# Kernel tuning notes

Measured on AMD Instinct MI355X. Metric: run time of the kernel, lower is better.

## Reference

```python
import jax, jax.numpy as jnp
import numpy as np

N_HEAD, D_MODEL, D_K, D_V = 16, 1024, 64, 64
B, S = 2, 2048
LN_EPS = 1e-5


def setup_inputs() -> dict:
    key = jax.random.key(0)
    ks = jax.random.split(key, 9)
    std_qk = np.sqrt(2.0 / (D_MODEL + D_K)).astype(np.float32)
    std_v = np.sqrt(2.0 / (D_MODEL + D_V)).astype(np.float32)
    return {
        "q": jax.random.normal(ks[0], (B, S, D_MODEL), jnp.float32),
        "k": jax.random.normal(ks[1], (B, S, D_MODEL), jnp.float32),
        "v": jax.random.normal(ks[2], (B, S, D_MODEL), jnp.float32),
        # nn.Linear weights stored as [out, in]; we apply x @ W.T
        "w_qs": jax.random.normal(ks[3], (N_HEAD * D_K, D_MODEL), jnp.float32) * std_qk,
        "w_ks": jax.random.normal(ks[4], (N_HEAD * D_K, D_MODEL), jnp.float32) * std_qk,
        "w_vs": jax.random.normal(ks[5], (N_HEAD * D_V, D_MODEL), jnp.float32) * std_v,
        "fc_w": jax.random.normal(ks[6], (D_MODEL, N_HEAD * D_V), jnp.float32) * np.sqrt(2.0 / (D_MODEL + N_HEAD * D_V)).astype(np.float32),
        "fc_b": jnp.zeros((D_MODEL,), jnp.float32),
        "ln_g": jnp.ones((D_MODEL,), jnp.float32),
        "ln_b": jnp.zeros((D_MODEL,), jnp.float32),
    }


def reference(q, k, v, w_qs, w_ks, w_vs, fc_w, fc_b, ln_g, ln_b):
    temperature = jnp.asarray(np.power(D_K, 0.5), q.dtype)
    residual = q
    # projections -> [b, s, h, d]
    qh = (q @ w_qs.T).reshape(B, S, N_HEAD, D_K)
    kh = (k @ w_ks.T).reshape(B, S, N_HEAD, D_K)
    vh = (v @ w_vs.T).reshape(B, S, N_HEAD, D_V)
    # scaled dot-product attention (dropout = identity in eval)
    attn = jnp.einsum('bqhd,bkhd->bhqk', qh, kh) / temperature
    attn = jax.nn.softmax(attn, axis=-1)  # (log_softmax in source is unused)
    out = jnp.einsum('bhqk,bkhd->bqhd', attn, vh).reshape(B, S, N_HEAD * D_V)
    out = out @ fc_w.T + fc_b
    # layer norm over last dim
    x = out + residual
    mu = jnp.mean(x, axis=-1, keepdims=True)
    var = jnp.var(x, axis=-1, keepdims=True)
    return (x - mu) * jax.lax.rsqrt(var + LN_EPS) * ln_g + ln_b
```

## Files before the change

### kernel.cpp

```cpp
#include <hip/hip_runtime.h>
#include <hip/hip_bf16.h>

typedef _Float16 f16x8 __attribute__((ext_vector_type(8)));
typedef _Float16 f16x4 __attribute__((ext_vector_type(4)));
typedef _Float16 f16x2 __attribute__((ext_vector_type(2)));
typedef float f32x4 __attribute__((ext_vector_type(4)));

#define DEVI __device__ __forceinline__

constexpr int S_LEN = 2048;
constexpr int DM    = 1024;
constexpr int NH    = 16;
constexpr int DHD   = 64;
constexpr int MTOT  = 2 * S_LEN;

DEVI f32x4 mfma16(f16x8 a, f16x8 b, f32x4 c) {
    return __builtin_amdgcn_mfma_f32_16x16x32_f16(a, b, c, 0, 0, 0);
}

DEVI f16x2 cvt_pk(float a, float b) {
    return __builtin_bit_cast(f16x2, __builtin_amdgcn_cvt_pkrtz(a, b));
}

DEVI float fexp2(float x) {
#if __has_builtin(__builtin_amdgcn_exp2f)
    return __builtin_amdgcn_exp2f(x);
#else
    return exp2f(x);
#endif
}

DEVI void gload_lds16(const _Float16* g, _Float16* l) {
    __builtin_amdgcn_global_load_lds(
        (const __attribute__((address_space(1))) void*)g,
        (__attribute__((address_space(3))) void*)l, 16, 0, 0);
}

__global__ void k_conv(const float* __restrict__ s0, const float* __restrict__ s1,
                       const float* __restrict__ s2, const float* __restrict__ s3,
                       const float* __restrict__ s4, const float* __restrict__ s5,
                       const float* __restrict__ s6,
                       _Float16* __restrict__ d0, _Float16* __restrict__ d1,
                       _Float16* __restrict__ d2, _Float16* __restrict__ d3,
                       _Float16* __restrict__ d4, _Float16* __restrict__ d5,
                       _Float16* __restrict__ d6)
{
    const int QN4 = (MTOT * DM) / 4;
    const int WN4 = (DM * DM) / 4;
    const int TOT = 3 * QN4 + 4 * WN4;
    int stride = gridDim.x * blockDim.x;
    for (int i = blockIdx.x * blockDim.x + threadIdx.x; i < TOT; i += stride) {
        const float* s; _Float16* d; int off;
        if (i < 3 * QN4) {
            int t = i / QN4; off = i - t * QN4;
            s = t == 0 ? s0 : (t == 1 ? s1 : s2);
            d = t == 0 ? d0 : (t == 1 ? d1 : d2);
        } else {
            int j = i - 3 * QN4;
            int t = j / WN4; off = j - t * WN4;
            s = t == 0 ? s3 : (t == 1 ? s4 : (t == 2 ? s5 : s6));
            d = t == 0 ? d3 : (t == 1 ? d4 : (t == 2 ? d5 : d6));
        }
        float4 v = reinterpret_cast<const float4*>(s)[off];
        f16x4 o;
        o[0] = (_Float16)v.x; o[1] = (_Float16)v.y;
        o[2] = (_Float16)v.z; o[3] = (_Float16)v.w;
        *reinterpret_cast<f16x4*>(d + (size_t)off * 4) = o;
    }
}

DEVI void gemm_main(const _Float16* __restrict__ A, const _Float16* __restrict__ Bw,
                    int kLen, int ld, int m0, int n0, f32x4 (&acc)[4][4])
{
    __shared__ __align__(16) _Float16 As[2][128 * 64];
    __shared__ __align__(16) _Float16 Bs[2][128 * 64];

    const int tid = threadIdx.x;
    const int lane = tid & 63;
    const int w = tid >> 6;
    const int wm = w >> 1, wn = w & 1;
    const int lrow = lane & 15, lg = lane >> 4;
    const int srow = w * 8 + (lane >> 3);
    const int scol = ((lane & 7) ^ (srow & 7)) * 8;

#pragma unroll
    for (int i = 0; i < 4; i++)
#pragma unroll
        for (int j = 0; j < 4; j++) acc[i][j] = f32x4{0.f, 0.f, 0.f, 0.f};

    const _Float16* gA = A  + (size_t)(m0 + srow) * ld + scol;
    const _Float16* gB = Bw + (size_t)(n0 + srow) * ld + scol;

#pragma unroll
    for (int q = 0; q < 4; q++) {
        gload_lds16(gA + (size_t)q * 32 * ld, &As[0][(w * 8 + q * 32) * 64]);
        gload_lds16(gB + (size_t)q * 32 * ld, &Bs[0][(w * 8 + q * 32) * 64]);
    }

    const int kTiles = kLen >> 6;
    for (int kt = 0; kt < kTiles; ++kt) {
        __syncthreads();
        if (kt + 1 < kTiles) {
            const int nb = (kt + 1) & 1;
            const int ko = (kt + 1) * 64;
#pragma unroll
            for (int q = 0; q < 4; q++) {
                gload_lds16(gA + ko + (size_t)q * 32 * ld, &As[nb][(w * 8 + q * 32) * 64]);
                gload_lds16(gB + ko + (size_t)q * 32 * ld, &Bs[nb][(w * 8 + q * 32) * 64]);
            }
        }
        const _Float16* Ab = As[kt & 1];
        const _Float16* Bb = Bs[kt & 1];
#pragma unroll
        for (int kk = 0; kk < 2; kk++) {
            f16x8 af[4], bfm[4];
#pragma unroll
            for (int i = 0; i < 4; i++) {
                int row = wm * 64 + i * 16 + lrow;
                int slot = (kk * 4 + lg) ^ (row & 7);
                af[i] = *reinterpret_cast<const f16x8*>(Ab + row * 64 + slot * 8);
            }
#pragma unroll
            for (int j = 0; j < 4; j++) {
                int row = wn * 64 + j * 16 + lrow;
                int slot = (kk * 4 + lg) ^ (row & 7);
                bfm[j] = *reinterpret_cast<const f16x8*>(Bb + row * 64 + slot * 8);
            }
#pragma unroll
            for (int i = 0; i < 4; i++)
#pragma unroll
                for (int j = 0; j < 4; j++)
                    acc[i][j] = mfma16(af[i], bfm[j], acc[i][j]);
        }
    }
}

__global__ __launch_bounds__(256, 2)
void k_proj(const _Float16* __restrict__ qb, const _Float16* __restrict__ kb,
            const _Float16* __restrict__ vb,
            const _Float16* __restrict__ wq, const _Float16* __restrict__ wk,
            const _Float16* __restrict__ wv,
            _Float16* __restrict__ Qh, _Float16* __restrict__ Kh, _Float16* __restrict__ Vt)
{
    const int z = blockIdx.z;
    const _Float16* A = z == 0 ? qb : (z == 1 ? kb : vb);
    const _Float16* B = z == 0 ? wq : (z == 1 ? wk : wv);
    const int m0 = blockIdx.x * 128, n0 = blockIdx.y * 128;
    f32x4 acc[4][4];
    gemm_main(A, B, DM, DM, m0, n0, acc);

    const int lane = threadIdx.x & 63, w = threadIdx.x >> 6;
    const int wm = w >> 1, wn = w & 1;
    const int lrow = lane & 15, lg = lane >> 4;

    if (z < 2) {
        _Float16* O = z == 0 ? Qh : Kh;
        const float scale = (z == 0) ? 0.18033688011112042f : 1.0f;
#pragma unroll
        for (int i = 0; i < 4; i++)
#pragma unroll
            for (int j = 0; j < 4; j++) {
                int n = n0 + wn * 64 + j * 16 + lrow;
                int h = n >> 6, d = n & 63;
#pragma unroll
                for (int r = 0; r < 4; r++) {
                    int m = m0 + wm * 64 + i * 16 + lg * 4 + r;
                    int b = m >> 11, s = m & (S_LEN - 1);
                    size_t idx = ((size_t)(b * NH + h) * S_LEN + s) * DHD + d;
                    O[idx] = (_Float16)(acc[i][j][r] * scale);
                }
            }
    } else {
#pragma unroll
        for (int i = 0; i < 4; i++) {
            int m = m0 + wm * 64 + i * 16 + lg * 4;
            int b = m >> 11, s = m & (S_LEN - 1);
#pragma unroll
            for (int j = 0; j < 4; j++) {
                int n = n0 + wn * 64 + j * 16 + lrow;
                int h = n >> 6, d = n & 63;
                size_t idx = ((size_t)(b * NH + h) * DHD + d) * S_LEN + s;
                f16x4 pk;
#pragma unroll
                for (int r = 0; r < 4; r++) pk[r] = (_Float16)acc[i][j][r];
                *reinterpret_cast<f16x4*>(Vt + idx) = pk;
            }
        }
    }
}

__global__ __launch_bounds__(256, 2)
void k_attn(const _Float16* __restrict__ Q, const _Float16* __restrict__ Kh,
            const _Float16* __restrict__ Vt, _Float16* __restrict__ Ob)
{
    __shared__ __align__(16) _Float16 Kl[2][64 * 64];
    __shared__ __align__(16) _Float16 Vl[2][64 * 64];
    __shared__ __align__(16) _Float16 Pl[4][32 * 64];

    const int tid  = threadIdx.x;
    const int lane = tid & 63, w = tid >> 6;
    const int lrow = lane & 15, lg = lane >> 4;

    const int raw  = blockIdx.x;
    const int swz  = (raw & 7) * 64 + (raw >> 3);
    const int bh   = swz >> 4;
    const int qblk = swz & 15;
    const int q0   = qblk * 128 + w * 32;

    const _Float16* Qb = Q  + (size_t)bh * S_LEN * DHD;
    const _Float16* Kb = Kh + (size_t)bh * S_LEN * DHD;
    const _Float16* Vb = Vt + (size_t)bh * DHD * S_LEN;

    f16x8 qf[2][2];
#pragma unroll
    for (int mi = 0; mi < 2; mi++)
#pragma unroll
        for (int ks = 0; ks < 2; ks++)
            qf[mi][ks] = *reinterpret_cast<const f16x8*>(
                Qb + (size_t)(q0 + mi * 16 + lrow) * DHD + ks * 32 + lg * 8);

    f32x4 oacc[2][4];
#pragma unroll
    for (int mi = 0; mi < 2; mi++)
#pragma unroll
        for (int df = 0; df < 4; df++) oacc[mi][df] = f32x4{0.f, 0.f, 0.f, 0.f};
    f32x4 lacc[2] = {f32x4{0.f, 0.f, 0.f, 0.f}, f32x4{0.f, 0.f, 0.f, 0.f}};

    f16x8 vones;
#pragma unroll
    for (int i = 0; i < 8; i++) vones[i] = (_Float16)1.0f;

    const int srow8 = lane >> 3, sslot = lane & 7;
    const _Float16* gK = Kb + (size_t)(w * 16 + srow8) * DHD   + sslot * 8;
    const _Float16* gV = Vb + (size_t)(w * 16 + srow8) * S_LEN + sslot * 8;
    const int lds_st = (w * 16 + srow8) * 64 + (sslot ^ srow8) * 8;

    f16x8 stK[2], stV[2];
#pragma unroll
    for (int i = 0; i < 2; i++) {
        stK[i] = *reinterpret_cast<const f16x8*>(gK + i * 8 * DHD);
        stV[i] = *reinterpret_cast<const f16x8*>(gV + i * 8 * S_LEN);
    }

    for (int t = 0; t < 32; ++t) {
        const int cur = t & 1;
        _Float16* Kc = Kl[cur];
        _Float16* Vc = Vl[cur];
#pragma unroll
        for (int i = 0; i < 2; i++) {
            *reinterpret_cast<f16x8*>(Kc + lds_st + i * 8 * 64) = stK[i];
            *reinterpret_cast<f16x8*>(Vc + lds_st + i * 8 * 64) = stV[i];
        }
        if (t + 1 < 32) {
#pragma unroll
            for (int i = 0; i < 2; i++) {
                stK[i] = *reinterpret_cast<const f16x8*>(gK + (size_t)(t + 1) * 64 * DHD + i * 8 * DHD);
                stV[i] = *reinterpret_cast<const f16x8*>(gV + (t + 1) * 64 + i * 8 * S_LEN);
            }
        }
        asm volatile("s_waitcnt lgkmcnt(0)" ::: "memory");
        __builtin_amdgcn_s_barrier();

#pragma unroll
        for (int kf = 0; kf < 4; kf++) {
            const int r = kf * 16 + lrow;
            f16x8 k0 = *reinterpret_cast<const f16x8*>(Kc + r * 64 + ((lg    ) ^ (r & 7)) * 8);
            f16x8 k1 = *reinterpret_cast<const f16x8*>(Kc + r * 64 + ((4 + lg) ^ (r & 7)) * 8);
            __builtin_amdgcn_s_setprio(1);
            f32x4 sc0 = mfma16(k0, qf[0][0], f32x4{-7.f, -7.f, -7.f, -7.f});
            sc0 = mfma16(k1, qf[0][1], sc0);
            f32x4 sc1 = mfma16(k0, qf[1][0], f32x4{-7.f, -7.f, -7.f, -7.f});
            sc1 = mfma16(k1, qf[1][1], sc1);
            __builtin_amdgcn_s_setprio(0);
            const int sl = (kf * 2 + (lg >> 1)) ^ (lrow & 7);
            {
                float p0 = fexp2(sc0[0]), p1 = fexp2(sc0[1]);
                float p2 = fexp2(sc0[2]), p3 = fexp2(sc0[3]);
                f16x4 hh = __builtin_shufflevector(cvt_pk(p0, p1), cvt_pk(p2, p3), 0, 1, 2, 3);
                *reinterpret_cast<f16x4*>(&Pl[w][lrow * 64 + sl * 8 + (lg & 1) * 4]) = hh;
            }
            {
                float p0 = fexp2(sc1[0]), p1 = fexp2(sc1[1]);
                float p2 = fexp2(sc1[2]), p3 = fexp2(sc1[3]);
                f16x4 hh = __builtin_shufflevector(cvt_pk(p0, p1), cvt_pk(p2, p3), 0, 1, 2, 3);
                *reinterpret_cast<f16x4*>(&Pl[w][(16 + lrow) * 64 + sl * 8 + (lg & 1) * 4]) = hh;
            }
        }

#pragma unroll
        for (int ks = 0; ks < 2; ks++) {
            const int psl = ((ks * 4 + lg) ^ (lrow & 7)) * 8;
            f16x8 pa0 = *reinterpret_cast<const f16x8*>(&Pl[w][lrow * 64 + psl]);
            f16x8 pa1 = *reinterpret_cast<const f16x8*>(&Pl[w][(16 + lrow) * 64 + psl]);
            __builtin_amdgcn_s_setprio(1);
#pragma unroll
            for (int df = 0; df < 4; df++) {
                const int r = df * 16 + lrow;
                f16x8 vf = *reinterpret_cast<const f16x8*>(Vc + r * 64 + ((ks * 4 + lg) ^ (r & 7)) * 8);
                oacc[0][df] = mfma16(pa0, vf, oacc[0][df]);
                oacc[1][df] = mfma16(pa1, vf, oacc[1][df]);
            }
            lacc[0] = mfma16(pa0, vones, lacc[0]);
            lacc[1] = mfma16(pa1, vones, lacc[1]);
            __builtin_amdgcn_s_setprio(0);
        }
    }

    const int b = bh >> 4, h = bh & 15;
#pragma unroll
    for (int mi = 0; mi < 2; mi++)
#pragma unroll
        for (int r = 0; r < 4; r++) {
            const float iq = 1.0f / lacc[mi][r];
            const int m = b * S_LEN + q0 + mi * 16 + lg * 4 + r;
#pragma unroll
            for (int df = 0; df < 4; df++)
                Ob[(size_t)m * DM + h * 64 + df * 16 + lrow] = (_Float16)(oacc[mi][df][r] * iq);
        }
}

__global__ __launch_bounds__(256, 2)
void k_fc(const _Float16* __restrict__ Ob, const _Float16* __restrict__ Wfc,
          const float* __restrict__ bias,
          _Float16* __restrict__ fcoA, _Float16* __restrict__ fcoB)
{
    const int z = blockIdx.z;
    const int m0 = blockIdx.x * 128, n0 = blockIdx.y * 128;
    f32x4 acc[4][4];
    gemm_main(Ob + z * 512, Wfc + z * 512, 512, DM, m0, n0, acc);

    _Float16* out = z == 0 ? fcoA : fcoB;
    const int lane = threadIdx.x & 63, w = threadIdx.x >> 6;
    const int wm = w >> 1, wn = w & 1;
    const int lrow = lane & 15, lg = lane >> 4;
#pragma unroll
    for (int j = 0; j < 4; j++) {
        int n = n0 + wn * 64 + j * 16 + lrow;
        float bv = (z == 0) ? bias[n] : 0.f;
#pragma unroll
        for (int i = 0; i < 4; i++)
#pragma unroll
            for (int r = 0; r < 4; r++) {
                int m = m0 + wm * 64 + i * 16 + lg * 4 + r;
                out[(size_t)m * DM + n] = (_Float16)(acc[i][j][r] + bv);
            }
    }
}

__global__ void k_ln(const _Float16* __restrict__ fa, const _Float16* __restrict__ fb,
                     const float* __restrict__ res,
                     const float* __restrict__ g, const float* __restrict__ be,
                     float* __restrict__ out)
{
    int row = blockIdx.x * 4 + (threadIdx.x >> 6);
    int lane = threadIdx.x & 63;
    const f16x4* ar = reinterpret_cast<const f16x4*>(fa + (size_t)row * DM);
    const f16x4* br2 = reinterpret_cast<const f16x4*>(fb + (size_t)row * DM);
    const float4* rr = reinterpret_cast<const float4*>(res + (size_t)row * DM);
    float4 v[4];
    float sum = 0.f, sq = 0.f;
#pragma unroll
    for (int t = 0; t < 4; t++) {
        f16x4 a = ar[lane + 64 * t];
        f16x4 bq = br2[lane + 64 * t];
        float4 b = rr[lane + 64 * t];
        float4 c = make_float4((float)a[0] + (float)bq[0] + b.x,
                               (float)a[1] + (float)bq[1] + b.y,
                               (float)a[2] + (float)bq[2] + b.z,
                               (float)a[3] + (float)bq[3] + b.w);
        v[t] = c;
        sum += c.x + c.y + c.z + c.w;
        sq  += c.x * c.x + c.y * c.y + c.z * c.z + c.w * c.w;
    }
#pragma unroll
    for (int o = 1; o < 64; o <<= 1) { sum += __shfl_xor(sum, o); sq += __shfl_xor(sq, o); }
    float mu = sum * (1.f / DM);
    float rstd = rsqrtf(fmaxf(sq * (1.f / DM) - mu * mu, 0.f) + 1e-5f);
    float4* orow = reinterpret_cast<float4*>(out + (size_t)row * DM);
    const float4* gr = reinterpret_cast<const float4*>(g);
    const float4* brr = reinterpret_cast<const float4*>(be);
#pragma unroll
    for (int t = 0; t < 4; t++) {
        float4 gg = gr[lane + 64 * t], bb = brr[lane + 64 * t];
        float4 c = v[t];
        orow[lane + 64 * t] = make_float4((c.x - mu) * rstd * gg.x + bb.x,
                                          (c.y - mu) * rstd * gg.y + bb.y,
                                          (c.z - mu) * rstd * gg.z + bb.z,
                                          (c.w - mu) * rstd * gg.w + bb.w);
    }
}

extern "C" void kernel_launch(void* const* d_in, const int* in_sizes, int n_in,
                              void* d_out, int out_size, void* d_ws, size_t ws_size,
                              hipStream_t stream)
{
    const float* q    = (const float*)d_in[0];
    const float* k    = (const float*)d_in[1];
    const float* v    = (const float*)d_in[2];
    const float* w_qs = (const float*)d_in[3];
    const float* w_ks = (const float*)d_in[4];
    const float* w_vs = (const float*)d_in[5];
    const float* fc_w = (const float*)d_in[6];
    const float* fc_b = (const float*)d_in[7];
    const float* ln_g = (const float*)d_in[8];
    const float* ln_b = (const float*)d_in[9];
    float* out = (float*)d_out;

    if (ws_size < (size_t)67108864) return;

    _Float16* ws  = (_Float16*)d_ws;
    _Float16* qbf = ws;
    _Float16* kbf = qbf + 4194304;
    _Float16* vbf = kbf + 4194304;
    _Float16* wq  = vbf + 4194304;
    _Float16* wk  = wq + 1048576;
    _Float16* wv  = wk + 1048576;
    _Float16* wfc = wv + 1048576;
    _Float16* Qh  = wfc + 1048576;
    _Float16* Kh  = Qh + 4194304;
    _Float16* Vt  = Kh + 4194304;
    _Float16* Ob  = Vt + 4194304;
    _Float16* fcoA = qbf;
    _Float16* fcoB = kbf;

    k_conv<<<2048, 256, 0, stream>>>(q, k, v, w_qs, w_ks, w_vs, fc_w,
                                     qbf, kbf, vbf, wq, wk, wv, wfc);
    k_proj<<<dim3(32, 8, 3), 256, 0, stream>>>(qbf, kbf, vbf, wq, wk, wv, Qh, Kh, Vt);
    k_attn<<<512, 256, 0, stream>>>(Qh, Kh, Vt, Ob);
    k_fc<<<dim3(32, 8, 2), 256, 0, stream>>>(Ob, wfc, fc_b, fcoA, fcoB);
    k_ln<<<1024, 256, 0, stream>>>(fcoA, fcoB, q, ln_g, ln_b, out);
}
```

Measured before the change: 133.5 us.

## Use 32x32 MFMA with register P via permlane swap; single-buffer GEMM LDS

The attention kernel moves from 16x16x32 MFMA to 32x32x16 MFMA and keeps the softmax probabilities in registers, using permlane32 swaps to reshape them into the A-operand layout. This removes the per-warp P round trip through shared memory. The GEMM helper drops double buffering to a single LDS buffer loaded after a barrier, and projection/fc launch bounds go to 4 blocks per CU for higher occupancy. In exchange, GEMM load latency is no longer overlapped with compute, which may offset the occupancy gain.

After: 123.6 us. -7.4%, faster.

```diff
diff --git a/kernel.cpp b/kernel.cpp
--- a/kernel.cpp
+++ b/kernel.cpp
@@ -5,6 +5,9 @@
 typedef _Float16 f16x4 __attribute__((ext_vector_type(4)));
 typedef _Float16 f16x2 __attribute__((ext_vector_type(2)));
 typedef float f32x4 __attribute__((ext_vector_type(4)));
+typedef float f32x16 __attribute__((ext_vector_type(16)));
+typedef unsigned u32x4v __attribute__((ext_vector_type(4)));
+typedef int i32x2 __attribute__((ext_vector_type(2)));
 
 #define DEVI __device__ __forceinline__
 
@@ -17,6 +20,9 @@
 DEVI f32x4 mfma16(f16x8 a, f16x8 b, f32x4 c) {
     return __builtin_amdgcn_mfma_f32_16x16x32_f16(a, b, c, 0, 0, 0);
 }
+DEVI f32x16 mfma32(f16x8 a, f16x8 b, f32x16 c) {
+    return __builtin_amdgcn_mfma_f32_32x32x16_f16(a, b, c, 0, 0, 0);
+}
 
 DEVI f16x2 cvt_pk(float a, float b) {
     return __builtin_bit_cast(f16x2, __builtin_amdgcn_cvt_pkrtz(a, b));
@@ -27,6 +33,22 @@
     return __builtin_amdgcn_exp2f(x);
 #else
     return exp2f(x);
+#endif
+}
+
+DEVI void pl32swap(unsigned &a, unsigned &b) {
+#if __has_builtin(__builtin_amdgcn_permlane32_swap)
+    i32x2 r = __builtin_bit_cast(i32x2,
+        __builtin_amdgcn_permlane32_swap((int)a, (int)b, false, false));
+    a = (unsigned)r[0]; b = (unsigned)r[1];
+#else
+    int idx = (((int)(threadIdx.x & 63)) ^ 32) << 2;
+    unsigned ra = (unsigned)__builtin_amdgcn_ds_bpermute(idx, (int)a);
+    unsigned rb = (unsigned)__builtin_amdgcn_ds_bpermute(idx, (int)b);
+    bool hi = (threadIdx.x & 32) != 0;
+    unsigned na = hi ? rb : a;
+    unsigned nb = hi ? b  : ra;
+    a = na; b = nb;
 #endif
 }
 
@@ -72,8 +94,8 @@
 DEVI void gemm_main(const _Float16* __restrict__ A, const _Float16* __restrict__ Bw,
                     int kLen, int ld, int m0, int n0, f32x4 (&acc)[4][4])
 {
-    __shared__ __align__(16) _Float16 As[2][128 * 64];
-    __shared__ __align__(16) _Float16 Bs[2][128 * 64];
+    __shared__ __align__(16) _Float16 As[128 * 64];
+    __shared__ __align__(16) _Float16 Bs[128 * 64];
 
     const int tid = threadIdx.x;
     const int lane = tid & 63;
@@ -93,24 +115,13 @@
 
 #pragma unroll
     for (int q = 0; q < 4; q++) {
-        gload_lds16(gA + (size_t)q * 32 * ld, &As[0][(w * 8 + q * 32) * 64]);
-        gload_lds16(gB + (size_t)q * 32 * ld, &Bs[0][(w * 8 + q * 32) * 64]);
+        gload_lds16(gA + (size_t)q * 32 * ld, &As[(w * 8 + q * 32) * 64]);
+        gload_lds16(gB + (size_t)q * 32 * ld, &Bs[(w * 8 + q * 32) * 64]);
     }
 
     const int kTiles = kLen >> 6;
     for (int kt = 0; kt < kTiles; ++kt) {
         __syncthreads();
-        if (kt + 1 < kTiles) {
-            const int nb = (kt + 1) & 1;
-            const int ko = (kt + 1) * 64;
-#pragma unroll
-            for (int q = 0; q < 4; q++) {
-                gload_lds16(gA + ko + (size_t)q * 32 * ld, &As[nb][(w * 8 + q * 32) * 64]);
-                gload_lds16(gB + ko + (size_t)q * 32 * ld, &Bs[nb][(w * 8 + q * 32) * 64]);
-            }
-        }
-        const _Float16* Ab = As[kt & 1];
-        const _Float16* Bb = Bs[kt & 1];
 #pragma unroll
         for (int kk = 0; kk < 2; kk++) {
             f16x8 af[4], bfm[4];
@@ -118,13 +129,13 @@
             for (int i = 0; i < 4; i++) {
                 int row = wm * 64 + i * 16 + lrow;
                 int slot = (kk * 4 + lg) ^ (row & 7);
-                af[i] = *reinterpret_cast<const f16x8*>(Ab + row * 64 + slot * 8);
+                af[i] = *reinterpret_cast<const f16x8*>(As + row * 64 + slot * 8);
             }
 #pragma unroll
             for (int j = 0; j < 4; j++) {
                 int row = wn * 64 + j * 16 + lrow;
                 int slot = (kk * 4 + lg) ^ (row & 7);
-                bfm[j] = *reinterpret_cast<const f16x8*>(Bb + row * 64 + slot * 8);
+                bfm[j] = *reinterpret_cast<const f16x8*>(Bs + row * 64 + slot * 8);
             }
 #pragma unroll
             for (int i = 0; i < 4; i++)
@@ -132,10 +143,20 @@
                 for (int j = 0; j < 4; j++)
                     acc[i][j] = mfma16(af[i], bfm[j], acc[i][j]);
         }
-    }
-}
-
-__global__ __launch_bounds__(256, 2)
+        if (kt + 1 < kTiles) {
+            asm volatile("s_waitcnt lgkmcnt(0)" ::: "memory");
+            __builtin_amdgcn_s_barrier();
+            const int ko = (kt + 1) * 64;
+#pragma unroll
+            for (int q = 0; q < 4; q++) {
+                gload_lds16(gA + ko + (size_t)q * 32 * ld, &As[(w * 8 + q * 32) * 64]);
+                gload_lds16(gB + ko + (size_t)q * 32 * ld, &Bs[(w * 8 + q * 32) * 64]);
+            }
+        }
+    }
+}
+
+__global__ __launch_bounds__(256, 4)
 void k_proj(const _Float16* __restrict__ qb, const _Float16* __restrict__ kb,
             const _Float16* __restrict__ vb,
             const _Float16* __restrict__ wq, const _Float16* __restrict__ wk,
@@ -195,11 +216,10 @@
 {
     __shared__ __align__(16) _Float16 Kl[2][64 * 64];
     __shared__ __align__(16) _Float16 Vl[2][64 * 64];
-    __shared__ __align__(16) _Float16 Pl[4][32 * 64];
 
     const int tid  = threadIdx.x;
     const int lane = tid & 63, w = tid >> 6;
-    const int lrow = lane & 15, lg = lane >> 4;
+    const int l31  = lane & 31, hh = lane >> 5;
 
     const int raw  = blockIdx.x;
     const int swz  = (raw & 7) * 64 + (raw >> 3);
@@ -211,21 +231,17 @@
     const _Float16* Kb = Kh + (size_t)bh * S_LEN * DHD;
     const _Float16* Vb = Vt + (size_t)bh * DHD * S_LEN;
 
-    f16x8 qf[2][2];
-#pragma unroll
-    for (int mi = 0; mi < 2; mi++)
-#pragma unroll
-        for (int ks = 0; ks < 2; ks++)
-            qf[mi][ks] = *reinterpret_cast<const f16x8*>(
-                Qb + (size_t)(q0 + mi * 16 + lrow) * DHD + ks * 32 + lg * 8);
-
-    f32x4 oacc[2][4];
-#pragma unroll
-    for (int mi = 0; mi < 2; mi++)
-#pragma unroll
-        for (int df = 0; df < 4; df++) oacc[mi][df] = f32x4{0.f, 0.f, 0.f, 0.f};
-    f32x4 lacc[2] = {f32x4{0.f, 0.f, 0.f, 0.f}, f32x4{0.f, 0.f, 0.f, 0.f}};
-
+    f16x8 qf[4];
+#pragma unroll
+    for (int step = 0; step < 4; step++)
+        qf[step] = *reinterpret_cast<const f16x8*>(
+            Qb + (size_t)(q0 + l31) * DHD + step * 16 + hh * 8);
+
+    f32x16 oacc[2], lacc, cinit;
+#pragma unroll
+    for (int i = 0; i < 16; i++) {
+        oacc[0][i] = 0.f; oacc[1][i] = 0.f; lacc[i] = 0.f; cinit[i] = -7.f;
+    }
     f16x8 vones;
 #pragma unroll
     for (int i = 0; i < 8; i++) vones[i] = (_Float16)1.0f;
@@ -261,65 +277,64 @@
         asm volatile("s_waitcnt lgkmcnt(0)" ::: "memory");
         __builtin_amdgcn_s_barrier();
 
-#pragma unroll
-        for (int kf = 0; kf < 4; kf++) {
-            const int r = kf * 16 + lrow;
-            f16x8 k0 = *reinterpret_cast<const f16x8*>(Kc + r * 64 + ((lg    ) ^ (r & 7)) * 8);
-            f16x8 k1 = *reinterpret_cast<const f16x8*>(Kc + r * 64 + ((4 + lg) ^ (r & 7)) * 8);
-            __builtin_amdgcn_s_setprio(1);
-            f32x4 sc0 = mfma16(k0, qf[0][0], f32x4{-7.f, -7.f, -7.f, -7.f});
-            sc0 = mfma16(k1, qf[0][1], sc0);
-            f32x4 sc1 = mfma16(k0, qf[1][0], f32x4{-7.f, -7.f, -7.f, -7.f});
-            sc1 = mfma16(k1, qf[1][1], sc1);
-            __builtin_amdgcn_s_setprio(0);
-            const int sl = (kf * 2 + (lg >> 1)) ^ (lrow & 7);
-            {
-                float p0 = fexp2(sc0[0]), p1 = fexp2(sc0[1]);
-                float p2 = fexp2(sc0[2]), p3 = fexp2(sc0[3]);
-                f16x4 hh = __builtin_shufflevector(cvt_pk(p0, p1), cvt_pk(p2, p3), 0, 1, 2, 3);
-                *reinterpret_cast<f16x4*>(&Pl[w][lrow * 64 + sl * 8 + (lg & 1) * 4]) = hh;
-            }
-            {
-                float p0 = fexp2(sc1[0]), p1 = fexp2(sc1[1]);
-                float p2 = fexp2(sc1[2]), p3 = fexp2(sc1[3]);
-                f16x4 hh = __builtin_shufflevector(cvt_pk(p0, p1), cvt_pk(p2, p3), 0, 1, 2, 3);
-                *reinterpret_cast<f16x4*>(&Pl[w][(16 + lrow) * 64 + sl * 8 + (lg & 1) * 4]) = hh;
-            }
-        }
-
-#pragma unroll
-        for (int ks = 0; ks < 2; ks++) {
-            const int psl = ((ks * 4 + lg) ^ (lrow & 7)) * 8;
-            f16x8 pa0 = *reinterpret_cast<const f16x8*>(&Pl[w][lrow * 64 + psl]);
-            f16x8 pa1 = *reinterpret_cast<const f16x8*>(&Pl[w][(16 + lrow) * 64 + psl]);
-            __builtin_amdgcn_s_setprio(1);
-#pragma unroll
-            for (int df = 0; df < 4; df++) {
-                const int r = df * 16 + lrow;
-                f16x8 vf = *reinterpret_cast<const f16x8*>(Vc + r * 64 + ((ks * 4 + lg) ^ (r & 7)) * 8);
-                oacc[0][df] = mfma16(pa0, vf, oacc[0][df]);
-                oacc[1][df] = mfma16(pa1, vf, oacc[1][df]);
-            }
-            lacc[0] = mfma16(pa0, vones, lacc[0]);
-            lacc[1] = mfma16(pa1, vones, lacc[1]);
-            __builtin_amdgcn_s_setprio(0);
+        f32x16 sc0 = cinit, sc1 = cinit;
+        __builtin_amdgcn_s_setprio(1);
+#pragma unroll
+        for (int step = 0; step < 4; step++) {
+            const int r0 = l31, r1 = 32 + l31;
+            const int sl = step * 2 + hh;
+            f16x8 ka = *reinterpret_cast<const f16x8*>(Kc + r0 * 64 + (sl ^ (r0 & 7)) * 8);
+            f16x8 kb = *reinterpret_cast<const f16x8*>(Kc + r1 * 64 + (sl ^ (r1 & 7)) * 8);
+            sc0 = mfma32(ka, qf[step], sc0);
+            sc1 = mfma32(kb, qf[step], sc1);
+        }
+        __builtin_amdgcn_s_setprio(0);
+
+#pragma unroll
+        for (int kb2 = 0; kb2 < 2; kb2++) {
+            const f32x16 sc = kb2 ? sc1 : sc0;
+            float e[16];
+#pragma unroll
+            for (int r = 0; r < 16; r++) e[r] = fexp2(sc[r]);
+            unsigned Wa[4], Wb[4];
+#pragma unroll
+            for (int g = 0; g < 4; g++) {
+                Wa[g] = __builtin_bit_cast(unsigned, cvt_pk(e[4 * g],     e[4 * g + 1]));
+                Wb[g] = __builtin_bit_cast(unsigned, cvt_pk(e[4 * g + 2], e[4 * g + 3]));
+            }
+            pl32swap(Wa[0], Wa[1]); pl32swap(Wb[0], Wb[1]);
+            pl32swap(Wa[2], Wa[3]); pl32swap(Wb[2], Wb[3]);
+#pragma unroll
+            for (int win = 0; win < 2; win++) {
+                u32x4v fw = {Wa[2 * win], Wb[2 * win], Wa[2 * win + 1], Wb[2 * win + 1]};
+                f16x8 pa = __builtin_bit_cast(f16x8, fw);
+                const int slotb = kb2 * 4 + win * 2 + hh;
+                __builtin_amdgcn_s_setprio(1);
+#pragma unroll
+                for (int dblk = 0; dblk < 2; dblk++) {
+                    const int row = dblk * 32 + l31;
+                    f16x8 vf = *reinterpret_cast<const f16x8*>(
+                        Vc + row * 64 + (slotb ^ (row & 7)) * 8);
+                    oacc[dblk] = mfma32(pa, vf, oacc[dblk]);
+                }
+                lacc = mfma32(pa, vones, lacc);
+                __builtin_amdgcn_s_setprio(0);
+            }
         }
     }
 
     const int b = bh >> 4, h = bh & 15;
 #pragma unroll
-    for (int mi = 0; mi < 2; mi++)
-#pragma unroll
-        for (int r = 0; r < 4; r++) {
-            const float iq = 1.0f / lacc[mi][r];
-            const int m = b * S_LEN + q0 + mi * 16 + lg * 4 + r;
-#pragma unroll
-            for (int df = 0; df < 4; df++)
-                Ob[(size_t)m * DM + h * 64 + df * 16 + lrow] = (_Float16)(oacc[mi][df][r] * iq);
-        }
-}
-
-__global__ __launch_bounds__(256, 2)
+    for (int r = 0; r < 16; r++) {
+        const float iq = 1.0f / lacc[r];
+        const int qrow = q0 + (r & 3) + 8 * (r >> 2) + 4 * hh;
+        const size_t m = (size_t)(b * S_LEN + qrow) * DM + h * 64;
+        Ob[m + l31]      = (_Float16)(oacc[0][r] * iq);
+        Ob[m + 32 + l31] = (_Float16)(oacc[1][r] * iq);
+    }
+}
+
+__global__ __launch_bounds__(256, 4)
 void k_fc(const _Float16* __restrict__ Ob, const _Float16* __restrict__ Wfc,
           const float* __restrict__ bias,
           _Float16* __restrict__ fcoA, _Float16* __restrict__ fcoB)
```
